# Kernel optimization log

Measured on AMD Instinct MI355X. Metric: run time of the kernel, lower is better.

The kernel has to match this reference:

```python
import jax, jax.numpy as jnp
import numpy as np

TWO_PI = 2.0 * np.pi


def setup_inputs() -> dict:
    key = jax.random.key(0)
    k1, k2, k3, k4 = jax.random.split(key, 4)
    N, H, W, B = 1024, 256, 256, 64
    pred = jax.random.uniform(k1, (N,), dtype=jnp.float32)
    mu = jax.random.uniform(k2, (N, 2), dtype=jnp.float32)              # centers in [0,1]
    sigma = jax.random.uniform(k3, (N, 2), dtype=jnp.float32) * 0.25 + 0.05  # widths in [0.05,0.30]
    nodes = jnp.concatenate([mu, sigma], axis=1)                         # [N,4]
    batch_list = jax.random.randint(k4, (N,), 0, B, dtype=jnp.int64)
    return {"pred": pred, "nodes": nodes, "batch_list": batch_list,
            "h": H, "w": W, "batch_num": B}


def reference(pred, nodes, batch_list, h, w, batch_num):
    # Normalized grid, identical to torch.arange(num)*step + start
    xs = jnp.linspace(0.0, 1.0, w, dtype=pred.dtype)   # [w]
    ys = jnp.linspace(0.0, 1.0, h, dtype=pred.dtype)   # [h]
    x_t = xs[None, :]                                   # broadcasts to [h,w]
    y_t = ys[:, None]

    mu_x = nodes[:, 0][:, None, None]
    mu_y = nodes[:, 1][:, None, None]
    sx = nodes[:, 2][:, None, None]
    sy = nodes[:, 3][:, None, None]

    # [N,h,w] per-node gaussian (epsilon = 0 in the original module)
    g = (1.0 / (TWO_PI * sx * sy)) * jnp.exp(
        -((x_t[None] - mu_x) ** 2 / (2.0 * sx ** 2)
          + (y_t[None] - mu_y) ** 2 / (2.0 * sy ** 2)))

    # normalize each node map by its max, scale by pred[i]
    g = g / jnp.max(g, axis=(1, 2), keepdims=True) * pred[:, None, None]

    # scatter-add into per-batch maps
    maps = jax.ops.segment_sum(g, batch_list, num_segments=batch_num)   # [B,h,w]
    return maps[:, None, :, :]                                          # [B,1,h,w]
```

## Files before the change

### kernel.cpp

```cpp
#include <hip/hip_runtime.h>
#include <math.h>

#define HCONST 256
#define WCONST 256
#define ROWS   32
#define TILES  (HCONST / ROWS)
#define CHUNK  64

__global__ __launch_bounds__(256) void fused_kernel(
    const float* __restrict__ pred,
    const float* __restrict__ nodes,
    const int*   __restrict__ batch_list,
    int N,
    float* __restrict__ out)
{
    const int b  = blockIdx.x / TILES;
    const int ty = blockIdx.x % TILES;
    const int y0 = ty * ROWS;
    const int t  = threadIdx.x;
    const int xi   = t & 127;
    const int half = t >> 7;

    __shared__ int    s_idx[1024];
    __shared__ int    s_cnt;
    __shared__ float4 s_prm[CHUNK];
    __shared__ float  s_fy[CHUNK][ROWS];

    if (t == 0) s_cnt = 0;
    __syncthreads();
    for (int n = t; n < N; n += 256) {
        if (batch_list[n] == b) {
            int p = atomicAdd(&s_cnt, 1);
            s_idx[p] = n;
        }
    }
    __syncthreads();
    const int cnt = s_cnt;

    const float step = 1.0f / 255.0f;
    const float x0s = (2 * xi)     * step;
    const float x1s = (2 * xi + 1) * step;

    float2 acc[16];
#pragma unroll
    for (int r = 0; r < 16; ++r) acc[r] = make_float2(0.0f, 0.0f);

    for (int c0 = 0; c0 < cnt; c0 += CHUNK) {
        const int cc = min(CHUNK, cnt - c0);

        for (int p = t; p < cc; p += 256) {
            const int n = s_idx[c0 + p];
            const float4 nd = ((const float4*)nodes)[n];
            const float ax = 1.0f / (2.0f * nd.z * nd.z);
            float ni = roundf(nd.x * 255.0f);
            ni = fminf(fmaxf(ni, 0.0f), 255.0f);
            const float dxm = ni * step - nd.x;
            s_prm[p] = make_float4(nd.x, ax, ax * dxm * dxm, 0.0f);
        }
        for (int it = t; it < cc * ROWS; it += 256) {
            const int g  = it >> 5;
            const int yy = it & 31;
            const int n  = s_idx[c0 + g];
            const float4 nd = ((const float4*)nodes)[n];
            const float ay = 1.0f / (2.0f * nd.w * nd.w);
            float ni = roundf(nd.y * 255.0f);
            ni = fminf(fmaxf(ni, 0.0f), 255.0f);
            const float dym = ni * step - nd.y;
            const float dy  = (y0 + yy) * step - nd.y;
            s_fy[g][yy] = pred[n] * __expf(ay * (dym * dym - dy * dy));
        }
        __syncthreads();

        for (int g = 0; g < cc; ++g) {
            const float4 prm = s_prm[g];
            const float dx0 = x0s - prm.x;
            const float dx1 = x1s - prm.x;
            const float e0 = __expf(prm.z - prm.y * dx0 * dx0);
            const float e1 = __expf(prm.z - prm.y * dx1 * dx1);
            const float4* fy4 = (const float4*)&s_fy[g][half * 16];
#pragma unroll
            for (int k = 0; k < 4; ++k) {
                const float4 f = fy4[k];
                acc[k*4+0].x = fmaf(f.x, e0, acc[k*4+0].x);
                acc[k*4+0].y = fmaf(f.x, e1, acc[k*4+0].y);
                acc[k*4+1].x = fmaf(f.y, e0, acc[k*4+1].x);
                acc[k*4+1].y = fmaf(f.y, e1, acc[k*4+1].y);
                acc[k*4+2].x = fmaf(f.z, e0, acc[k*4+2].x);
                acc[k*4+2].y = fmaf(f.z, e1, acc[k*4+2].y);
                acc[k*4+3].x = fmaf(f.w, e0, acc[k*4+3].x);
                acc[k*4+3].y = fmaf(f.w, e1, acc[k*4+3].y);
            }
        }
        __syncthreads();
    }

    float* o = out + ((size_t)b * HCONST + y0 + half * 16) * WCONST + 2 * xi;
#pragma unroll
    for (int r = 0; r < 16; ++r)
        ((float2*)(o + (size_t)r * WCONST))[0] = acc[r];
}

extern "C" void kernel_launch(void* const* d_in, const int* in_sizes, int n_in,
                              void* d_out, int out_size, void* d_ws, size_t ws_size,
                              hipStream_t stream) {
    const float* pred       = (const float*)d_in[0];
    const float* nodes      = (const float*)d_in[1];
    const int*   batch_list = (const int*)d_in[2];

    const int N = in_sizes[0];
    const int B = out_size / (HCONST * WCONST);

    float* out = (float*)d_out;

    fused_kernel<<<B * TILES, 256, 0, stream>>>(pred, nodes, batch_list, N, out);
}
```

Baseline: 74.12 us.

## Enlarge per-thread tile to 16x4 pixels with 64-row block tiles

Each block now covers 64 rows instead of 32, and each thread computes 4 adjacent x pixels across 16 rows, so it holds 64 float4-packed accumulators. Every loaded fy value now feeds four FMAs, x-exponentials are shared across more rows, and stores become float4. The grid is halved to B*4 blocks (256 blocks at B=64), and each thread uses more registers. That may reduce occupancy and leave part of the GPU's compute units idle.

```diff
diff --git a/kernel.cpp b/kernel.cpp
--- a/kernel.cpp
+++ b/kernel.cpp
@@ -3,7 +3,7 @@
 
 #define HCONST 256
 #define WCONST 256
-#define ROWS   32
+#define ROWS   64
 #define TILES  (HCONST / ROWS)
 #define CHUNK  64
 
@@ -18,8 +18,8 @@
     const int ty = blockIdx.x % TILES;
     const int y0 = ty * ROWS;
     const int t  = threadIdx.x;
-    const int xi   = t & 127;
-    const int half = t >> 7;
+    const int xi = t & 63;
+    const int q  = t >> 6;
 
     __shared__ int    s_idx[1024];
     __shared__ int    s_cnt;
@@ -38,12 +38,14 @@
     const int cnt = s_cnt;
 
     const float step = 1.0f / 255.0f;
-    const float x0s = (2 * xi)     * step;
-    const float x1s = (2 * xi + 1) * step;
+    const float xs0 = (4 * xi)     * step;
+    const float xs1 = (4 * xi + 1) * step;
+    const float xs2 = (4 * xi + 2) * step;
+    const float xs3 = (4 * xi + 3) * step;
 
-    float2 acc[16];
+    float4 acc[16];
 #pragma unroll
-    for (int r = 0; r < 16; ++r) acc[r] = make_float2(0.0f, 0.0f);
+    for (int r = 0; r < 16; ++r) acc[r] = make_float4(0.f, 0.f, 0.f, 0.f);
 
     for (int c0 = 0; c0 < cnt; c0 += CHUNK) {
         const int cc = min(CHUNK, cnt - c0);
@@ -58,8 +60,8 @@
             s_prm[p] = make_float4(nd.x, ax, ax * dxm * dxm, 0.0f);
         }
         for (int it = t; it < cc * ROWS; it += 256) {
-            const int g  = it >> 5;
-            const int yy = it & 31;
+            const int g  = it >> 6;
+            const int yy = it & 63;
             const int n  = s_idx[c0 + g];
             const float4 nd = ((const float4*)nodes)[n];
             const float ay = 1.0f / (2.0f * nd.w * nd.w);
@@ -73,31 +75,37 @@
 
         for (int g = 0; g < cc; ++g) {
             const float4 prm = s_prm[g];
-            const float dx0 = x0s - prm.x;
-            const float dx1 = x1s - prm.x;
+            const float dx0 = xs0 - prm.x;
+            const float dx1 = xs1 - prm.x;
+            const float dx2 = xs2 - prm.x;
+            const float dx3 = xs3 - prm.x;
             const float e0 = __expf(prm.z - prm.y * dx0 * dx0);
             const float e1 = __expf(prm.z - prm.y * dx1 * dx1);
-            const float4* fy4 = (const float4*)&s_fy[g][half * 16];
+            const float e2 = __expf(prm.z - prm.y * dx2 * dx2);
+            const float e3 = __expf(prm.z - prm.y * dx3 * dx3);
+            const float4* fy4 = (const float4*)&s_fy[g][q * 16];
 #pragma unroll
             for (int k = 0; k < 4; ++k) {
                 const float4 f = fy4[k];
-                acc[k*4+0].x = fmaf(f.x, e0, acc[k*4+0].x);
-                acc[k*4+0].y = fmaf(f.x, e1, acc[k*4+0].y);
-                acc[k*4+1].x = fmaf(f.y, e0, acc[k*4+1].x);
-                acc[k*4+1].y = fmaf(f.y, e1, acc[k*4+1].y);
-                acc[k*4+2].x = fmaf(f.z, e0, acc[k*4+2].x);
-                acc[k*4+2].y = fmaf(f.z, e1, acc[k*4+2].y);
-                acc[k*4+3].x = fmaf(f.w, e0, acc[k*4+3].x);
-                acc[k*4+3].y = fmaf(f.w, e1, acc[k*4+3].y);
+#pragma unroll
+                for (int j = 0; j < 4; ++j) {
+                    const float fv = (j == 0) ? f.x : (j == 1) ? f.y
+                                   : (j == 2) ? f.z : f.w;
+                    float4& a = acc[k * 4 + j];
+                    a.x = fmaf(fv, e0, a.x);
+                    a.y = fmaf(fv, e1, a.y);
+                    a.z = fmaf(fv, e2, a.z);
+                    a.w = fmaf(fv, e3, a.w);
+                }
             }
         }
         __syncthreads();
     }
 
-    float* o = out + ((size_t)b * HCONST + y0 + half * 16) * WCONST + 2 * xi;
+    float* o = out + ((size_t)b * HCONST + y0 + q * 16) * WCONST + 4 * xi;
 #pragma unroll
     for (int r = 0; r < 16; ++r)
-        ((float2*)(o + (size_t)r * WCONST))[0] = acc[r];
+        ((float4*)(o + (size_t)r * WCONST))[0] = acc[r];
 }
 
 extern "C" void kernel_launch(void* const* d_in, const int* in_sizes, int n_in,
```

After: 74.62 us. Within noise of the previous version (+0.7%).
